# Kernel tuning notes

Measured on AMD Instinct MI355X. Metric: run time of the kernel, lower is better.

The kernel has to match this reference:

```python
import jax, jax.numpy as jnp
import numpy as np

B, C, H, W = 8, 128, 64, 64
K = 3
MID = C // 4  # reduction=4


def setup_inputs() -> dict:
    key = jax.random.key(0)
    ks = jax.random.split(key, 8)
    f = lambda k, s, sc=1.0: jax.random.normal(k, s, dtype=jnp.float32) * sc
    return {
        "X2": f(ks[0], (B, C, H, W)),
        "Y2": f(ks[1], (B, C, H, W)),
        "static_w": f(ks[2], (C, 1, K, K), 0.1),        # depthwise conv weight (OIHW, groups=C)
        "w1": f(ks[3], (2 * MID, 2 * C), 0.05),          # context_conv1 1x1
        "w2": f(ks[4], (2 * MID, 2 * MID), 0.05),        # context_conv2 1x1
        "w3": f(ks[5], (C * K * K, 2 * MID), 0.05),      # context_conv3 1x1
        "ws": f(ks[6], (K * K, 2 * C), 0.05),            # spatial_conv 1x1
        "wf": f(ks[7], (C, 2 * C), 0.05),                # fusion_conv 1x1
    }


def _c1x1(w, x):
    # 1x1 conv, no bias: (O,I) x (B,I,H,W) -> (B,O,H,W)
    return jnp.einsum('oc,bchw->bohw', w, x)


def reference(X2, Y2, static_w, w1, w2, w3, ws, wf):
    Bn, Cn, Hn, Wn = X2.shape
    Kn = static_w.shape[-1]
    pad = (Kn - 1) // 2

    # static depthwise conv
    Xs = jax.lax.conv_general_dilated(
        X2, static_w, window_strides=(1, 1), padding='SAME',
        feature_group_count=Cn, dimension_numbers=('NCHW', 'OIHW', 'NCHW'))

    Fc = jnp.concatenate([Xs, Y2], axis=1)  # (B, 2C, H, W)

    # SE-style context branch: 1x1 conv -> global avg pool -> 1x1 -> relu -> 1x1
    ctx = _c1x1(w1, Fc).mean(axis=(2, 3))                  # (B, 2*mid)
    ctx = jax.nn.relu(jnp.einsum('oc,bc->bo', w2, ctx))    # (B, 2*mid)
    channel_filter = jnp.einsum('oc,bc->bo', w3, ctx)      # (B, C*k*k)
    channel_filter = channel_filter.reshape(Bn, Cn, Kn * Kn, 1, 1)

    spatial_filter = _c1x1(ws, Fc).reshape(Bn, 1, Kn * Kn, Hn, Wn)
    dynamic_filter = channel_filter + spatial_filter       # (B, C, k*k, H, W)

    # unfold X2: patch order matches F.unfold (channel-major, kernel row-major)
    Xp = jnp.pad(X2, ((0, 0), (0, 0), (pad, pad), (pad, pad)))
    patches = jnp.stack(
        [Xp[:, :, i:i + Hn, j:j + Wn] for i in range(Kn) for j in range(Kn)],
        axis=2)                                            # (B, C, k*k, H, W)

    dynamic_out = (patches * dynamic_filter).sum(axis=2)   # (B, C, H, W)

    out = _c1x1(wf, jnp.concatenate([Xs, dynamic_out], axis=1))
    return out
```

## Files before the change

### kernel.cpp

```cpp
#include <hip/hip_runtime.h>
#include <hip/hip_bf16.h>

#define Bn 8
#define Cn 128
#define Hn 64
#define Wn 64
#define HWn 4096
#define KK 9

typedef short short8 __attribute__((ext_vector_type(8)));
typedef float f32x4 __attribute__((ext_vector_type(4)));

__device__ inline unsigned short f2b(float v) {
    __hip_bfloat16 h = __float2bfloat16(v);
    return *reinterpret_cast<unsigned short*>(&h);
}

__global__ __launch_bounds__(256) void k_pre(
    const float* __restrict__ X2, const float* __restrict__ Y2,
    float* __restrict__ pws)
{
    int bc = blockIdx.x, t = threadIdx.x;
    const float4* xp = (const float4*)(X2 + (size_t)bc * HWn);
    const float4* yp = (const float4*)(Y2 + (size_t)bc * HWn);
    float v[10];
#pragma unroll
    for (int k = 0; k < 10; k++) v[k] = 0.f;
#pragma unroll
    for (int i = 0; i < 4; i++) {
        int q = t + i * 256;
        float4 x = xp[q], y = yp[q];
        float s4 = x.x + x.y + x.z + x.w;
        v[0] += s4;
        v[5] += y.x + y.y + y.z + y.w;
        int px = q * 4, h = px >> 6, w4 = px & 63;
        if (h == 0)   v[1] += s4;
        if (h == 63)  v[2] += s4;
        if (w4 == 0)  v[3] += x.x;
        if (w4 == 60) v[4] += x.w;
        if (px == 0)    v[6] += x.x;
        if (px == 60)   v[7] += x.w;
        if (px == 4032) v[8] += x.x;
        if (px == 4092) v[9] += x.w;
    }
#pragma unroll
    for (int k = 0; k < 10; k++)
#pragma unroll
        for (int off = 32; off; off >>= 1)
            v[k] += __shfl_down(v[k], off);
    __shared__ float red[4][10];
    int lane = t & 63, wv = t >> 6;
    if (lane == 0) {
#pragma unroll
        for (int k = 0; k < 10; k++) red[wv][k] = v[k];
    }
    __syncthreads();
    if (t < 10) pws[bc * 10 + t] = red[0][t] + red[1][t] + red[2][t] + red[3][t];
}

__global__ __launch_bounds__(256) void k_ctx(
    const float* __restrict__ pws, const float* __restrict__ sw,
    const float* __restrict__ w1, const float* __restrict__ w2,
    const float* __restrict__ w3, const float* __restrict__ wf,
    const float* __restrict__ wsp, float* __restrict__ cf,
    unsigned short* __restrict__ wfb, unsigned short* __restrict__ wsb)
{
    int blk = blockIdx.x, b = blk >> 2, qd = blk & 3;
    int t = threadIdx.x;
    for (int i = t; i < 1024; i += 256) {
        int j = blk * 1024 + i;
        wfb[j] = f2b(wf[j]);
    }
    {
        int j = blk * 128 + t;
        if (t < 128) {
            int tt = j >> 8, c = j & 255;
            wsb[j] = (tt < KK) ? f2b(wsp[tt * 256 + c]) : (unsigned short)0;
        }
    }
    __shared__ float mfc[256], c1[64], c2[64];
    if (t < 128) {
        const float* S = pws + (b * Cn + t) * 10;
        float T = S[0];
        float R[3]  = { S[2], 0.f, S[1] };
        float Cc[3] = { S[4], 0.f, S[3] };
        float Xc[3][3] = {{S[9], 0.f, S[8]}, {0.f, 0.f, 0.f}, {S[7], 0.f, S[6]}};
        float a = 0.f;
#pragma unroll
        for (int i = 0; i < 3; i++)
#pragma unroll
            for (int j = 0; j < 3; j++)
                a += sw[t * 9 + i * 3 + j] * (T - R[i] - Cc[j] + Xc[i][j]);
        mfc[t] = a * (1.f / HWn);
    } else {
        mfc[t] = pws[(b * Cn + (t - 128)) * 10 + 5] * (1.f / HWn);
    }
    __syncthreads();
    if (t < 64) {
        const float4* wr = (const float4*)(w1 + t * 256);
        float a = 0.f;
        for (int c = 0; c < 64; c++) {
            float4 v = wr[c];
            a += v.x * mfc[c*4] + v.y * mfc[c*4+1] + v.z * mfc[c*4+2] + v.w * mfc[c*4+3];
        }
        c1[t] = a;
    }
    __syncthreads();
    if (t < 64) {
        const float4* wr = (const float4*)(w2 + t * 64);
        float a = 0.f;
        for (int c = 0; c < 16; c++) {
            float4 v = wr[c];
            a += v.x * c1[c*4] + v.y * c1[c*4+1] + v.z * c1[c*4+2] + v.w * c1[c*4+3];
        }
        c2[t] = fmaxf(a, 0.f);
    }
    __syncthreads();
    for (int j = qd * 288 + t; j < qd * 288 + 288; j += 256) {
        const float4* wr = (const float4*)(w3 + j * 64);
        float a = 0.f;
        for (int c = 0; c < 16; c++) {
            float4 v = wr[c];
            a += v.x * c2[c*4] + v.y * c2[c*4+1] + v.z * c2[c*4+2] + v.w * c2[c*4+3];
        }
        cf[b * Cn * KK + j] = a;
    }
}

__global__ __launch_bounds__(512, 2) void k_main(
    const float* __restrict__ X2, const float* __restrict__ Y2,
    const float* __restrict__ sw,
    const unsigned short* __restrict__ wfb, const unsigned short* __restrict__ wsb,
    const float* __restrict__ cf, float* __restrict__ out)
{
    __shared__ unsigned short sFt[2][Wn][Cn];
    __shared__ float sSf[KK][Wn];
    __shared__ float sCfP[Cn][12];
    __shared__ float sSwP[Cn][12];

    int bid = blockIdx.x;
    int b = bid & 7, h = bid >> 3;
    int t = threadIdx.x;
    int w = t & 63, cg = t >> 6;
    int swz = (w & 7) << 3;
    int c0 = cg * 16;

    for (int i = t; i < Cn * KK; i += 512) {
        int c = i / 9, q = i - c * 9;
        sSwP[c][q] = sw[i];
        sCfP[c][q] = cf[b * Cn * KK + i];
    }

    const float* xcol = X2 + (size_t)(b * Cn + c0) * HWn + h * Wn + w;
    const float* ycol = Y2 + (size_t)(b * Cn + c0) * HWn + h * Wn + w;
    bool hm = h > 0, hp = h < Hn - 1;
    bool wm = w > 0, wp = w < Wn - 1;

    float tap[16][3];
    float yv[16];

#pragma unroll
    for (int i = 0; i < 16; i++) {
        const float* xp = xcol + (size_t)i * HWn;
        tap[i][0] = hm ? xp[-Wn] : 0.f;
        tap[i][1] = xp[0];
        tap[i][2] = hp ? xp[Wn] : 0.f;
        yv[i] = __builtin_nontemporal_load(ycol + (size_t)i * HWn);
    }
    __syncthreads();

    {
        unsigned int px[4], py[4];
#pragma unroll
        for (int i = 0; i < 16; i++) {
            int c = c0 + i;
            float r0 = tap[i][0], r1 = tap[i][1], r2 = tap[i][2];
            float4 k0 = *(const float4*)&sSwP[c][0];
            float4 k1 = *(const float4*)&sSwP[c][4];
            float  k8 = sSwP[c][8];
            float xl0 = __shfl_up(r0, 1), xr0 = __shfl_down(r0, 1);
            float xl1 = __shfl_up(r1, 1), xr1 = __shfl_down(r1, 1);
            float xl2 = __shfl_up(r2, 1), xr2 = __shfl_down(r2, 1);
            if (!wm) { xl0 = 0.f; xl1 = 0.f; xl2 = 0.f; }
            if (!wp) { xr0 = 0.f; xr1 = 0.f; xr2 = 0.f; }
            float a = k0.x * xl0 + k0.y * r0 + k0.z * xr0
                    + k0.w * xl1 + k1.x * r1 + k1.y * xr1
                    + k1.z * xl2 + k1.w * r2 + k8 * xr2;
            unsigned int ah = f2b(a), yh = f2b(yv[i]);
            int sub = i & 7;
            if ((sub & 1) == 0) { px[sub >> 1] = ah; py[sub >> 1] = yh; }
            else { px[sub >> 1] |= ah << 16; py[sub >> 1] |= yh << 16; }
            if (sub == 7) {
                int col = (c - 7) ^ swz;
                *(uint4*)(&sFt[0][w][col]) = *(uint4*)px;
                *(uint4*)(&sFt[1][w][col]) = *(uint4*)py;
            }
        }
    }
    __syncthreads();

    {
        int lane = t & 63, wv = t >> 6;
        int l16 = lane & 15, half = lane >> 4, kk = half * 8;
        if (wv < 4) {
            int wA = wv * 16 + l16;
            int swzA = (wA & 7) << 3;
            f32x4 acc = (f32x4){0.f, 0.f, 0.f, 0.f};
#pragma unroll
            for (int ks = 0; ks < 8; ks++) {
                short8 av = *(const short8*)(wsb + l16 * 256 + ks * 32 + kk);
                int col = (((ks & 3) * 32 + kk)) ^ swzA;
                short8 bv = *(const short8*)(&sFt[ks >> 2][wA][0] + col);
                acc = __builtin_amdgcn_mfma_f32_16x16x32_bf16(av, bv, acc, 0, 0, 0);
            }
#pragma unroll
            for (int r = 0; r < 4; r++) {
                int tt = half * 4 + r;
                if (tt < KK) sSf[tt][wA] = acc[r];
            }
        }
    }
    __syncthreads();

    {
        float sfw[9];
#pragma unroll
        for (int q = 0; q < 9; q++) sfw[q] = sSf[q][w];
        unsigned int pd[4];
#pragma unroll
        for (int i = 0; i < 16; i++) {
            int c = c0 + i;
            float r0 = tap[i][0], r1 = tap[i][1], r2 = tap[i][2];
            float4 e0 = *(const float4*)&sCfP[c][0];
            float4 e1 = *(const float4*)&sCfP[c][4];
            float  e8 = sCfP[c][8];
            float xl0 = __shfl_up(r0, 1), xr0 = __shfl_down(r0, 1);
            float xl1 = __shfl_up(r1, 1), xr1 = __shfl_down(r1, 1);
            float xl2 = __shfl_up(r2, 1), xr2 = __shfl_down(r2, 1);
            if (!wm) { xl0 = 0.f; xl1 = 0.f; xl2 = 0.f; }
            if (!wp) { xr0 = 0.f; xr1 = 0.f; xr2 = 0.f; }
            float a = (e0.x + sfw[0]) * xl0 + (e0.y + sfw[1]) * r0 + (e0.z + sfw[2]) * xr0
                    + (e0.w + sfw[3]) * xl1 + (e1.x + sfw[4]) * r1 + (e1.y + sfw[5]) * xr1
                    + (e1.z + sfw[6]) * xl2 + (e1.w + sfw[7]) * r2 + (e8 + sfw[8]) * xr2;
            unsigned int ah = f2b(a);
            int sub = i & 7;
            if ((sub & 1) == 0) pd[sub >> 1] = ah;
            else pd[sub >> 1] |= ah << 16;
            if (sub == 7) {
                int col = (c - 7) ^ swz;
                *(uint4*)(&sFt[1][w][col]) = *(uint4*)pd;
            }
        }
    }
    __syncthreads();

    {
        int lane = t & 63, wv = t >> 6;
        int l16 = lane & 15, half = lane >> 4, kk = half * 8;
        int o0 = wv * 16;
        f32x4 acc[4];
#pragma unroll
        for (int n = 0; n < 4; n++) acc[n] = (f32x4){0.f, 0.f, 0.f, 0.f};
#pragma unroll
        for (int ks = 0; ks < 8; ks++) {
            int bufi = ks >> 2;
            int kc = (ks & 3) * 32 + kk;
            short8 av = *(const short8*)(wfb + (o0 + l16) * 256 + ks * 32 + kk);
#pragma unroll
            for (int n = 0; n < 4; n++) {
                int wB = n * 16 + l16;
                int col = kc ^ ((wB & 7) << 3);
                short8 bv = *(const short8*)(&sFt[bufi][wB][0] + col);
                acc[n] = __builtin_amdgcn_mfma_f32_16x16x32_bf16(av, bv, acc[n], 0, 0, 0);
            }
        }
        size_t obase = (size_t)b * Cn * HWn + (size_t)h * Wn;
#pragma unroll
        for (int n = 0; n < 4; n++)
#pragma unroll
            for (int r = 0; r < 4; r++) {
                int o = o0 + half * 4 + r;
                __builtin_nontemporal_store(
                    acc[n][r], &out[obase + (size_t)o * HWn + n * 16 + l16]);
            }
    }
}

extern "C" void kernel_launch(void* const* d_in, const int* in_sizes, int n_in,
                              void* d_out, int out_size, void* d_ws, size_t ws_size,
                              hipStream_t stream) {
    (void)in_sizes; (void)n_in; (void)out_size; (void)ws_size;
    const float* X2  = (const float*)d_in[0];
    const float* Y2  = (const float*)d_in[1];
    const float* sw  = (const float*)d_in[2];
    const float* w1  = (const float*)d_in[3];
    const float* w2  = (const float*)d_in[4];
    const float* w3  = (const float*)d_in[5];
    const float* wsp = (const float*)d_in[6];
    const float* wf  = (const float*)d_in[7];
    float* out = (float*)d_out;

    float* wsf = (float*)d_ws;
    float* pws = wsf;
    float* cf  = wsf + 10240;
    unsigned short* wfb = (unsigned short*)(wsf + 19456);
    unsigned short* wsb = (unsigned short*)(wsf + 35840);

    hipLaunchKernelGGL(k_pre, dim3(Bn * Cn), dim3(256), 0, stream, X2, Y2, pws);
    hipLaunchKernelGGL(k_ctx, dim3(32), dim3(256), 0, stream,
                       pws, sw, w1, w2, w3, wf, wsp, cf, wfb, wsb);
    hipLaunchKernelGGL(k_main, dim3(Bn * Hn), dim3(512), 0, stream,
                       X2, Y2, sw, wfb, wsb, cf, out);
}
```

Measured before the change: 49.69 us.

## Fold depthwise and channel filters into per-tap fusion-conv GEMMs with spatial-filter pass

Rewrites the maths so the static depthwise conv and the per-batch channel-filter conv are folded into the fusion conv weights (per-tap combined matrices Cb built in k_ctx). k_main now runs a 9-tap implicit GEMM over X2 with MFMA, computes wf·X2 (U) and the spatial filter via a folded Db matrix. A new k_fin kernel applies the per-pixel spatial filter to U and adds the GEMM result. This trades the scalar depthwise/dynamic-conv work for about nine times more MFMA work, bf16 intermediates in global memory (Tb, U), and an extra kernel launch.

```diff
diff --git a/kernel.cpp b/kernel.cpp
--- a/kernel.cpp
+++ b/kernel.cpp
@@ -14,6 +14,9 @@
 __device__ inline unsigned short f2b(float v) {
     __hip_bfloat16 h = __float2bfloat16(v);
     return *reinterpret_cast<unsigned short*>(&h);
+}
+__device__ inline float b2f(unsigned short u) {
+    return __uint_as_float(((unsigned int)u) << 16);
 }
 
 __global__ __launch_bounds__(256) void k_pre(
@@ -62,8 +65,9 @@
     const float* __restrict__ pws, const float* __restrict__ sw,
     const float* __restrict__ w1, const float* __restrict__ w2,
     const float* __restrict__ w3, const float* __restrict__ wf,
-    const float* __restrict__ wsp, float* __restrict__ cf,
-    unsigned short* __restrict__ wfb, unsigned short* __restrict__ wsb)
+    const float* __restrict__ wsp,
+    unsigned short* __restrict__ wfb, unsigned short* __restrict__ wsb,
+    unsigned short* __restrict__ Cb, unsigned short* __restrict__ Db)
 {
     int blk = blockIdx.x, b = blk >> 2, qd = blk & 3;
     int t = threadIdx.x;
@@ -71,14 +75,17 @@
         int j = blk * 1024 + i;
         wfb[j] = f2b(wf[j]);
     }
-    {
+    if (t < 128) {
         int j = blk * 128 + t;
-        if (t < 128) {
-            int tt = j >> 8, c = j & 255;
-            wsb[j] = (tt < KK) ? f2b(wsp[tt * 256 + c]) : (unsigned short)0;
-        }
-    }
+        int tt = j >> 8, c = j & 255;
+        wsb[j] = (tt < KK) ? f2b(wsp[tt * 256 + c]) : (unsigned short)0;
+    }
+
     __shared__ float mfc[256], c1[64], c2[64];
+    __shared__ float scf[Cn][KK];
+    __shared__ float ssw[Cn][KK];
+    for (int j = t; j < Cn * KK; j += 256) ssw[j / 9][j % 9] = sw[j];
+
     if (t < 128) {
         const float* S = pws + (b * Cn + t) * 10;
         float T = S[0];
@@ -116,173 +123,225 @@
         c2[t] = fmaxf(a, 0.f);
     }
     __syncthreads();
-    for (int j = qd * 288 + t; j < qd * 288 + 288; j += 256) {
+    for (int j = t; j < Cn * KK; j += 256) {
         const float4* wr = (const float4*)(w3 + j * 64);
         float a = 0.f;
         for (int c = 0; c < 16; c++) {
             float4 v = wr[c];
             a += v.x * c2[c*4] + v.y * c2[c*4+1] + v.z * c2[c*4+2] + v.w * c2[c*4+3];
         }
-        cf[b * Cn * KK + j] = a;
+        scf[j / 9][j % 9] = a;
+    }
+    __syncthreads();
+
+    {
+        int o = qd * 32 + (t >> 3);
+        int cb = (t & 7) * 16;
+        float wx[16], wd[16];
+#pragma unroll
+        for (int j = 0; j < 16; j++) {
+            wx[j] = wf[o * 256 + cb + j];
+            wd[j] = wf[o * 256 + 128 + cb + j];
+        }
+#pragma unroll
+        for (int tt = 0; tt < 9; tt++) {
+            unsigned short tmp[16];
+#pragma unroll
+            for (int j = 0; j < 16; j++) {
+                int c = cb + j;
+                tmp[j] = f2b(wx[j] * ssw[c][tt] + wd[j] * scf[c][tt]);
+            }
+            unsigned short* dst = Cb + (((size_t)b * 9 + tt) * Cn + o) * Cn + cb;
+            *(uint4*)(dst)     = ((uint4*)tmp)[0];
+            *(uint4*)(dst + 8) = ((uint4*)tmp)[1];
+        }
+    }
+    if (blk == 0 && t < 128) {
+        int s = t >> 3, cb = (t & 7) * 16;
+#pragma unroll
+        for (int tt = 0; tt < 9; tt++) {
+            unsigned short tmp[16];
+#pragma unroll
+            for (int j = 0; j < 16; j++) {
+                int c = cb + j;
+                float v = (s < KK) ? wsp[s * 256 + c] * ssw[c][tt] : 0.f;
+                tmp[j] = f2b(v);
+            }
+            unsigned short* dst = Db + ((size_t)tt * 16 + s) * Cn + cb;
+            *(uint4*)(dst)     = ((uint4*)tmp)[0];
+            *(uint4*)(dst + 8) = ((uint4*)tmp)[1];
+        }
     }
 }
 
 __global__ __launch_bounds__(512, 2) void k_main(
     const float* __restrict__ X2, const float* __restrict__ Y2,
-    const float* __restrict__ sw,
+    const unsigned short* __restrict__ Cb, const unsigned short* __restrict__ Db,
     const unsigned short* __restrict__ wfb, const unsigned short* __restrict__ wsb,
-    const float* __restrict__ cf, float* __restrict__ out)
+    unsigned short* __restrict__ Tb, unsigned short* __restrict__ U,
+    float* __restrict__ sfB)
 {
-    __shared__ unsigned short sFt[2][Wn][Cn];
-    __shared__ float sSf[KK][Wn];
-    __shared__ float sCfP[Cn][12];
-    __shared__ float sSwP[Cn][12];
-
+    __shared__ unsigned short sB[3][66][Cn];
+    __shared__ unsigned short sY[Wn][Cn];
+
+    int bid = blockIdx.x, b = bid & 7, h = bid >> 3;
+    int t = threadIdx.x;
+
+    for (int idx = t; idx < 768; idx += 512) {
+        int r = idx / 256, side = (idx >> 7) & 1, c = idx & 127;
+        sB[r][side ? 65 : 0][c] = 0;
+    }
+    for (int u = t; u < 6144; u += 512) {
+        int w4 = u & 15, rc = u >> 4;
+        int r = rc % 3, c = rc / 3;
+        int hh = h - 1 + r;
+        float4 v = (hh >= 0 && hh < Hn)
+            ? *(const float4*)(X2 + ((size_t)(b * Cn + c) * HWn + hh * Wn + w4 * 4))
+            : (float4){0.f, 0.f, 0.f, 0.f};
+        float va[4] = { v.x, v.y, v.z, v.w };
+#pragma unroll
+        for (int j = 0; j < 4; j++) {
+            int wpos = w4 * 4 + j + 1;
+            sB[r][wpos][c ^ (((wpos >> 1) & 7) << 3)] = f2b(va[j]);
+        }
+    }
+    for (int u = t; u < 2048; u += 512) {
+        int w4 = u & 15, c = u >> 4;
+        float4 v = *(const float4*)(Y2 + ((size_t)(b * Cn + c) * HWn + h * Wn + w4 * 4));
+        float va[4] = { v.x, v.y, v.z, v.w };
+#pragma unroll
+        for (int j = 0; j < 4; j++) {
+            int w = w4 * 4 + j;
+            sY[w][c ^ (((w >> 1) & 7) << 3)] = f2b(va[j]);
+        }
+    }
+    __syncthreads();
+
+    int lane = t & 63, wv = t >> 6;
+    int l16 = lane & 15, half = lane >> 4, kk = half * 8;
+
+    if (wv < 4) {
+        int o0 = wv * 32;
+        const unsigned short* Cbase = Cb + (size_t)b * 9 * Cn * Cn;
+        f32x4 acc[2][4];
+#pragma unroll
+        for (int m = 0; m < 2; m++)
+#pragma unroll
+            for (int n = 0; n < 4; n++)
+                acc[m][n] = (f32x4){0.f, 0.f, 0.f, 0.f};
+#pragma unroll
+        for (int tap = 0; tap < 9; tap++) {
+            const int dh = tap / 3, dw = tap % 3;
+#pragma unroll
+            for (int ks = 0; ks < 4; ks++) {
+                short8 av0 = *(const short8*)(Cbase + ((size_t)tap * Cn + o0 + l16) * Cn + ks * 32 + kk);
+                short8 av1 = *(const short8*)(Cbase + ((size_t)tap * Cn + o0 + 16 + l16) * Cn + ks * 32 + kk);
+#pragma unroll
+                for (int n = 0; n < 4; n++) {
+                    int wpos = n * 16 + l16 + dw;
+                    int col = (ks * 32 + kk) ^ (((wpos >> 1) & 7) << 3);
+                    short8 bv = *(const short8*)(&sB[dh][wpos][col]);
+                    acc[0][n] = __builtin_amdgcn_mfma_f32_16x16x32_bf16(av0, bv, acc[0][n], 0, 0, 0);
+                    acc[1][n] = __builtin_amdgcn_mfma_f32_16x16x32_bf16(av1, bv, acc[1][n], 0, 0, 0);
+                }
+            }
+        }
+#pragma unroll
+        for (int m = 0; m < 2; m++)
+#pragma unroll
+            for (int n = 0; n < 4; n++)
+#pragma unroll
+                for (int r = 0; r < 4; r++) {
+                    int o = o0 + m * 16 + half * 4 + r;
+                    Tb[(size_t)(b * Cn + o) * HWn + h * Wn + n * 16 + l16] = f2b(acc[m][n][r]);
+                }
+    } else {
+        int n = wv - 4;
+        int px = n * 16 + l16;
+        f32x4 accu[8];
+#pragma unroll
+        for (int m = 0; m < 8; m++) accu[m] = (f32x4){0.f, 0.f, 0.f, 0.f};
+        {
+            int wpos = px + 1;
+#pragma unroll
+            for (int ks = 0; ks < 4; ks++) {
+                int col = (ks * 32 + kk) ^ (((wpos >> 1) & 7) << 3);
+                short8 bv = *(const short8*)(&sB[1][wpos][col]);
+#pragma unroll
+                for (int m = 0; m < 8; m++) {
+                    short8 av = *(const short8*)(wfb + (m * 16 + l16) * 256 + 128 + ks * 32 + kk);
+                    accu[m] = __builtin_amdgcn_mfma_f32_16x16x32_bf16(av, bv, accu[m], 0, 0, 0);
+                }
+            }
+        }
+#pragma unroll
+        for (int m = 0; m < 8; m++)
+#pragma unroll
+            for (int r = 0; r < 4; r++) {
+                int o = m * 16 + half * 4 + r;
+                U[(size_t)(b * Cn + o) * HWn + h * Wn + px] = f2b(accu[m][r]);
+            }
+        f32x4 accs = (f32x4){0.f, 0.f, 0.f, 0.f};
+#pragma unroll
+        for (int tap = 0; tap < 9; tap++) {
+            const int dh = tap / 3, dw = tap % 3;
+            int wpos = px + dw;
+#pragma unroll
+            for (int ks = 0; ks < 4; ks++) {
+                int col = (ks * 32 + kk) ^ (((wpos >> 1) & 7) << 3);
+                short8 bv = *(const short8*)(&sB[dh][wpos][col]);
+                short8 av = *(const short8*)(Db + ((size_t)tap * 16 + l16) * Cn + ks * 32 + kk);
+                accs = __builtin_amdgcn_mfma_f32_16x16x32_bf16(av, bv, accs, 0, 0, 0);
+            }
+        }
+#pragma unroll
+        for (int ks = 0; ks < 4; ks++) {
+            int col = (ks * 32 + kk) ^ (((px >> 1) & 7) << 3);
+            short8 bv = *(const short8*)(&sY[px][col]);
+            short8 av = *(const short8*)(wsb + l16 * 256 + 128 + ks * 32 + kk);
+            accs = __builtin_amdgcn_mfma_f32_16x16x32_bf16(av, bv, accs, 0, 0, 0);
+        }
+#pragma unroll
+        for (int r = 0; r < 4; r++) {
+            int tt = half * 4 + r;
+            if (tt < KK)
+                sfB[((size_t)b * KK + tt) * HWn + h * Wn + px] = accs[r];
+        }
+    }
+}
+
+__global__ __launch_bounds__(512) void k_fin(
+    const unsigned short* __restrict__ U, const unsigned short* __restrict__ Tb,
+    const float* __restrict__ sfB, float* __restrict__ out)
+{
     int bid = blockIdx.x;
     int b = bid & 7, h = bid >> 3;
     int t = threadIdx.x;
-    int w = t & 63, cg = t >> 6;
-    int swz = (w & 7) << 3;
-    int c0 = cg * 16;
-
-    for (int i = t; i < Cn * KK; i += 512) {
-        int c = i / 9, q = i - c * 9;
-        sSwP[c][q] = sw[i];
-        sCfP[c][q] = cf[b * Cn * KK + i];
-    }
-
-    const float* xcol = X2 + (size_t)(b * Cn + c0) * HWn + h * Wn + w;
-    const float* ycol = Y2 + (size_t)(b * Cn + c0) * HWn + h * Wn + w;
+    int w = t & 63, og = t >> 6;
     bool hm = h > 0, hp = h < Hn - 1;
-    bool wm = w > 0, wp = w < Wn - 1;
-
-    float tap[16][3];
-    float yv[16];
-
+
+    float sfw[9];
+#pragma unroll
+    for (int q = 0; q < 9; q++)
+        sfw[q] = sfB[(size_t)(b * KK + q) * HWn + h * Wn + w];
+
+    size_t base = (size_t)(b * Cn + og * 16) * HWn + h * Wn + w;
 #pragma unroll
     for (int i = 0; i < 16; i++) {
-        const float* xp = xcol + (size_t)i * HWn;
-        tap[i][0] = hm ? xp[-Wn] : 0.f;
-        tap[i][1] = xp[0];
-        tap[i][2] = hp ? xp[Wn] : 0.f;
-        yv[i] = __builtin_nontemporal_load(ycol + (size_t)i * HWn);
-    }
-    __syncthreads();
-
-    {
-        unsigned int px[4], py[4];
-#pragma unroll
-        for (int i = 0; i < 16; i++) {
-            int c = c0 + i;
-            float r0 = tap[i][0], r1 = tap[i][1], r2 = tap[i][2];
-            float4 k0 = *(const float4*)&sSwP[c][0];
-            float4 k1 = *(const float4*)&sSwP[c][4];
-            float  k8 = sSwP[c][8];
-            float xl0 = __shfl_up(r0, 1), xr0 = __shfl_down(r0, 1);
-            float xl1 = __shfl_up(r1, 1), xr1 = __shfl_down(r1, 1);
-            float xl2 = __shfl_up(r2, 1), xr2 = __shfl_down(r2, 1);
-            if (!wm) { xl0 = 0.f; xl1 = 0.f; xl2 = 0.f; }
-            if (!wp) { xr0 = 0.f; xr1 = 0.f; xr2 = 0.f; }
-            float a = k0.x * xl0 + k0.y * r0 + k0.z * xr0
-                    + k0.w * xl1 + k1.x * r1 + k1.y * xr1
-                    + k1.z * xl2 + k1.w * r2 + k8 * xr2;
-            unsigned int ah = f2b(a), yh = f2b(yv[i]);
-            int sub = i & 7;
-            if ((sub & 1) == 0) { px[sub >> 1] = ah; py[sub >> 1] = yh; }
-            else { px[sub >> 1] |= ah << 16; py[sub >> 1] |= yh << 16; }
-            if (sub == 7) {
-                int col = (c - 7) ^ swz;
-                *(uint4*)(&sFt[0][w][col]) = *(uint4*)px;
-                *(uint4*)(&sFt[1][w][col]) = *(uint4*)py;
-            }
-        }
-    }
-    __syncthreads();
-
-    {
-        int lane = t & 63, wv = t >> 6;
-        int l16 = lane & 15, half = lane >> 4, kk = half * 8;
-        if (wv < 4) {
-            int wA = wv * 16 + l16;
-            int swzA = (wA & 7) << 3;
-            f32x4 acc = (f32x4){0.f, 0.f, 0.f, 0.f};
-#pragma unroll
-            for (int ks = 0; ks < 8; ks++) {
-                short8 av = *(const short8*)(wsb + l16 * 256 + ks * 32 + kk);
-                int col = (((ks & 3) * 32 + kk)) ^ swzA;
-                short8 bv = *(const short8*)(&sFt[ks >> 2][wA][0] + col);
-                acc = __builtin_amdgcn_mfma_f32_16x16x32_bf16(av, bv, acc, 0, 0, 0);
-            }
-#pragma unroll
-            for (int r = 0; r < 4; r++) {
-                int tt = half * 4 + r;
-                if (tt < KK) sSf[tt][wA] = acc[r];
-            }
-        }
-    }
-    __syncthreads();
-
-    {
-        float sfw[9];
-#pragma unroll
-        for (int q = 0; q < 9; q++) sfw[q] = sSf[q][w];
-        unsigned int pd[4];
-#pragma unroll
-        for (int i = 0; i < 16; i++) {
-            int c = c0 + i;
-            float r0 = tap[i][0], r1 = tap[i][1], r2 = tap[i][2];
-            float4 e0 = *(const float4*)&sCfP[c][0];
-            float4 e1 = *(const float4*)&sCfP[c][4];
-            float  e8 = sCfP[c][8];
-            float xl0 = __shfl_up(r0, 1), xr0 = __shfl_down(r0, 1);
-            float xl1 = __shfl_up(r1, 1), xr1 = __shfl_down(r1, 1);
-            float xl2 = __shfl_up(r2, 1), xr2 = __shfl_down(r2, 1);
-            if (!wm) { xl0 = 0.f; xl1 = 0.f; xl2 = 0.f; }
-            if (!wp) { xr0 = 0.f; xr1 = 0.f; xr2 = 0.f; }
-            float a = (e0.x + sfw[0]) * xl0 + (e0.y + sfw[1]) * r0 + (e0.z + sfw[2]) * xr0
-                    + (e0.w + sfw[3]) * xl1 + (e1.x + sfw[4]) * r1 + (e1.y + sfw[5]) * xr1
-                    + (e1.z + sfw[6]) * xl2 + (e1.w + sfw[7]) * r2 + (e8 + sfw[8]) * xr2;
-            unsigned int ah = f2b(a);
-            int sub = i & 7;
-            if ((sub & 1) == 0) pd[sub >> 1] = ah;
-            else pd[sub >> 1] |= ah << 16;
-            if (sub == 7) {
-                int col = (c - 7) ^ swz;
-                *(uint4*)(&sFt[1][w][col]) = *(uint4*)pd;
-            }
-        }
-    }
-    __syncthreads();
-
-    {
-        int lane = t & 63, wv = t >> 6;
-        int l16 = lane & 15, half = lane >> 4, kk = half * 8;
-        int o0 = wv * 16;
-        f32x4 acc[4];
-#pragma unroll
-        for (int n = 0; n < 4; n++) acc[n] = (f32x4){0.f, 0.f, 0.f, 0.f};
-#pragma unroll
-        for (int ks = 0; ks < 8; ks++) {
-            int bufi = ks >> 2;
-            int kc = (ks & 3) * 32 + kk;
-            short8 av = *(const short8*)(wfb + (o0 + l16) * 256 + ks * 32 + kk);
-#pragma unroll
-            for (int n = 0; n < 4; n++) {
-                int wB = n * 16 + l16;
-                int col = kc ^ ((wB & 7) << 3);
-                short8 bv = *(const short8*)(&sFt[bufi][wB][0] + col);
-                acc[n] = __builtin_amdgcn_mfma_f32_16x16x32_bf16(av, bv, acc[n], 0, 0, 0);
-            }
-        }
-        size_t obase = (size_t)b * Cn * HWn + (size_t)h * Wn;
-#pragma unroll
-        for (int n = 0; n < 4; n++)
-#pragma unroll
-            for (int r = 0; r < 4; r++) {
-                int o = o0 + half * 4 + r;
-                __builtin_nontemporal_store(
-                    acc[n][r], &out[obase + (size_t)o * HWn + n * 16 + l16]);
-            }
+        const unsigned short* up = U + base + (size_t)i * HWn;
+        float r0 = hm ? b2f(up[-Wn]) : 0.f;
+        float r1 = b2f(up[0]);
+        float r2 = hp ? b2f(up[Wn]) : 0.f;
+        float xl0 = __shfl_up(r0, 1), xr0 = __shfl_down(r0, 1);
+        float xl1 = __shfl_up(r1, 1), xr1 = __shfl_down(r1, 1);
+        float xl2 = __shfl_up(r2, 1), xr2 = __shfl_down(r2, 1);
+        if (w == 0)  { xl0 = 0.f; xl1 = 0.f; xl2 = 0.f; }
+        if (w == 63) { xr0 = 0.f; xr1 = 0.f; xr2 = 0.f; }
+        float a = sfw[0] * xl0 + sfw[1] * r0 + sfw[2] * xr0
+                + sfw[3] * xl1 + sfw[4] * r1 + sfw[5] * xr1
+                + sfw[6] * xl2 + sfw[7] * r2 + sfw[8] * xr2;
+        a += b2f(Tb[base + (size_t)i * HWn]);
+        __builtin_nontemporal_store(a, &out[base + (size_t)i * HWn]);
     }
 }
 
@@ -301,14 +360,20 @@
     float* out = (float*)d_out;
 
     float* wsf = (float*)d_ws;
-    float* pws = wsf;
-    float* cf  = wsf + 10240;
-    unsigned short* wfb = (unsigned short*)(wsf + 19456);
-    unsigned short* wsb = (unsigned short*)(wsf + 35840);
+    unsigned short* Tb = (unsigned short*)wsf;
+    unsigned short* U  = (unsigned short*)(wsf + 2097152);
+    float* sfB = wsf + 4194304;
+    float* pws = wsf + 4489216;
+    unsigned short* wfb = (unsigned short*)(wsf + 4499456);
+    unsigned short* wsb = (unsigned short*)(wsf + 4515840);
+    unsigned short* Cb  = (unsigned short*)(wsf + 4517888);
+    unsigned short* Db  = (unsigned short*)(wsf + 5107712);
 
     hipLaunchKernelGGL(k_pre, dim3(Bn * Cn), dim3(256), 0, stream, X2, Y2, pws);
     hipLaunchKernelGGL(k_ctx, dim3(32), dim3(256), 0, stream,
-                       pws, sw, w1, w2, w3, wf, wsp, cf, wfb, wsb);
+                       pws, sw, w1, w2, w3, wf, wsp, wfb, wsb, Cb, Db);
     hipLaunchKernelGGL(k_main, dim3(Bn * Hn), dim3(512), 0, stream,
-                       X2, Y2, sw, wfb, wsb, cf, out);
-}
+                       X2, Y2, Cb, Db, wfb, wsb, Tb, U, sfB);
+    hipLaunchKernelGGL(k_fin, dim3(Bn * Hn), dim3(512), 0, stream,
+                       U, Tb, sfB, out);
+}
```

Result: slower. 103.7 us (+108.7%).
